# Kernel optimization log

Measured on AMD Instinct MI355X. Metric: run time of the kernel, lower is better.

Reference implementation:

```python
import jax, jax.numpy as jnp
import numpy as np

N_ATOMS = 16384
N_EDGES = 524288
N_MOL = 256
A = 4            # num_pseudo_species
S = 4            # len(unique_numbers)
NMAX = 10        # radial basis size
NSPH = 9         # (l_max+1)^2 with l_max=2
Q = A * NMAX
NL = 3           # l_max+1
F = Q * Q * NL   # 4800 power-spectrum features
CUTOFF = 5.0
AVG_ATOMS = 64.0
SCALE = 1.0
H1, H2 = 512, 512


def _sph_l012(u):
    # real spherical harmonics l=0,1,2 on unit vectors u [E,3] -> [E,9]
    x, y, z = u[:, 0], u[:, 1], u[:, 2]
    c1 = 0.4886025119029199
    c2 = 1.0925484305920792
    return jnp.stack([
        jnp.full_like(x, 0.28209479177387814),
        c1 * y, c1 * z, c1 * x,
        c2 * x * y, c2 * y * z,
        0.31539156525252005 * (3.0 * z * z - 1.0),
        c2 * x * z,
        0.5462742152960396 * (x * x - y * y),
    ], axis=-1)


def _forward(positions, cells, edge_offsets, U, gamma, beta, W1, W2, W3, Wc,
             numbers, edge_indices, batch):
    send, recv = edge_indices[0], edge_indices[1]
    cell_e = cells[batch[send]]                                  # [E,3,3]
    rvec = positions[recv] - positions[send] + jnp.einsum('ek,ekl->el', edge_offsets, cell_e)
    r = jnp.sqrt(jnp.sum(rvec * rvec, axis=-1) + 1e-12)          # [E]
    rhat = rvec / r[:, None]
    fc = 0.5 * (jnp.cos(jnp.pi * r / CUTOFF) + 1.0) * (r < CUTOFF)
    mu = jnp.linspace(0.0, CUTOFF, NMAX)
    sig = CUTOFF / NMAX
    R = jnp.exp(-((r[:, None] - mu) ** 2) / (2.0 * sig * sig)) * fc[:, None]  # [E,NMAX]
    Y = _sph_l012(rhat)                                          # [E,9]
    RY = jnp.einsum('en,ek->enk', R, Y)                          # [E,NMAX,9]
    w = U[:, numbers[send]]                                      # [A,E] pseudo-species mix of neighbor species
    # spherical expansion per atom: c[i,a,n,lm]
    c = jnp.stack([jax.ops.segment_sum(w[a][:, None, None] * RY, recv, num_segments=N_ATOMS)
                   for a in range(A)], axis=1)                   # [N,A,NMAX,9]
    c = c.reshape(N_ATOMS, Q, NSPH)
    # power spectrum: contract over m within each l block, normalize by sqrt(2l+1)
    lblocks = [(0, 1, 1.0), (1, 4, 3.0), (4, 9, 5.0)]
    ps = jnp.stack([jnp.einsum('iqm,ipm->iqp', c[:, :, a:b], c[:, :, a:b]) / jnp.sqrt(nl)
                    for a, b, nl in lblocks], axis=-1).reshape(N_ATOMS, F)
    # layer norm
    mean = ps.mean(axis=-1, keepdims=True)
    var = ps.var(axis=-1, keepdims=True)
    x = (ps - mean) / jnp.sqrt(var + 1e-5) * gamma + beta

    def contract(x, W):
        # species-indexed contraction: per-species weight via combination matrix U
        Wsp = jnp.einsum('as,aio->sio', U, W)                    # [S,in,out]
        out = jnp.zeros((x.shape[0], W.shape[-1]), x.dtype)
        for s in range(S):                                       # small fixed species set
            out = out + jnp.where((numbers == s)[:, None], x @ Wsp[s], 0.0)
        return out

    x = jax.nn.silu(contract(x, W1))
    x = jax.nn.silu(contract(x, W2))
    x = contract(x, W3)                                          # [N,1]
    e = jax.ops.segment_sum(x, batch, num_segments=N_MOL)        # [M,1]
    e = e / jnp.sqrt(float(A)) / AVG_ATOMS
    comp = jax.ops.segment_sum(jax.nn.one_hot(numbers, S, dtype=x.dtype), batch, num_segments=N_MOL)
    return e * SCALE + comp @ Wc.T


def setup_inputs() -> dict:
    key = jax.random.key(0)
    ks = jax.random.split(key, 10)
    positions = jax.random.normal(ks[0], (N_ATOMS, 3), dtype=jnp.float32)
    cells = jnp.zeros((N_MOL, 3, 3), dtype=jnp.float32)
    numbers = jax.random.randint(ks[1], (N_ATOMS,), 0, S)
    edge_indices = jax.random.randint(ks[2], (2, N_EDGES), 0, N_ATOMS)
    edge_offsets = jnp.zeros((N_EDGES, 3), dtype=jnp.float32)
    batch = jnp.sort(jax.random.randint(ks[3], (N_ATOMS,), 0, N_MOL))
    U = jax.random.normal(ks[4], (A, S), dtype=jnp.float32) * 0.5
    gamma = jnp.ones((F,), dtype=jnp.float32)
    beta = jnp.zeros((F,), dtype=jnp.float32)
    W1 = jax.random.normal(ks[5], (A, F, H1), dtype=jnp.float32) / np.sqrt(F)
    W2 = jax.random.normal(ks[6], (A, H1, H2), dtype=jnp.float32) / np.sqrt(H1)
    W3 = jax.random.normal(ks[7], (A, H2, 1), dtype=jnp.float32) / np.sqrt(H2)
    Wc = jax.random.normal(ks[8], (1, S), dtype=jnp.float32) * 0.1
    return {"positions": positions, "cells": cells, "numbers": numbers,
            "edge_indices": edge_indices, "edge_offsets": edge_offsets, "batch": batch,
            "U": U, "gamma": gamma, "beta": beta, "W1": W1, "W2": W2, "W3": W3, "Wc": Wc}


def reference(positions, cells, numbers, edge_indices, edge_offsets, batch,
              U, gamma, beta, W1, W2, W3, Wc):
    return _forward(positions, cells, edge_offsets, U, gamma, beta, W1, W2, W3, Wc,
                    numbers, edge_indices, batch)
```

## Files before the change

kernel.cpp:

```cpp
#include <hip/hip_runtime.h>

#define NA   16384
#define NE   524288
#define NM   256
#define FF   4800
#define FR   2688
#define HH   512
#define NMX  10
#define NSPH 9

typedef __bf16 bf16x8 __attribute__((ext_vector_type(8)));
typedef float  f32x4  __attribute__((ext_vector_type(4)));
typedef unsigned short u16x8 __attribute__((ext_vector_type(8)));

__device__ inline unsigned short f2bf(float x){
  unsigned int u = __builtin_bit_cast(unsigned int, x);
  u += 0x7fffu + ((u >> 16) & 1u);
  return (unsigned short)(u >> 16);
}
__device__ inline float bf2f(unsigned short h){
  unsigned int u = ((unsigned int)h) << 16;
  return __builtin_bit_cast(float, u);
}
__device__ inline void atomic_add_f(float* p, float v){
  __hip_atomic_fetch_add(p, v, __ATOMIC_RELAXED, __HIP_MEMORY_SCOPE_AGENT);
}
__device__ inline void gload16(const void* g, void* l){
  __builtin_amdgcn_global_load_lds(
      (const __attribute__((address_space(1))) unsigned int*)g,
      (__attribute__((address_space(3))) unsigned int*)l, 16, 0, 0);
}
__device__ inline float silu(float x){ return x / (1.f + __expf(-x)); }

__device__ inline void decode_blk(int b, int& qb, int& pb){
  int q = 0, rem = b;
  while (rem >= 10 - q){ rem -= 10 - q; q++; }
  qb = q; pb = q + rem;
}

template<int CNT>
__device__ inline void ps_block(const float* __restrict__ cl, int qb, int pb, int off,
                                float nrm, bool diag, unsigned short* ob,
                                float& s1, float& s2){
  float cq[4][CNT], cp[4][CNT];
  #pragma unroll
  for (int i = 0; i < 4; i++)
    #pragma unroll
    for (int k = 0; k < CNT; k++){
      cq[i][k] = cl[(qb*4 + i)*9 + off + k];
      cp[i][k] = cl[(pb*4 + i)*9 + off + k];
    }
  #pragma unroll
  for (int qi = 0; qi < 4; qi++)
    #pragma unroll
    for (int pi = 0; pi < 4; pi++){
      float v = 0.f;
      #pragma unroll
      for (int k = 0; k < CNT; k++) v += cq[qi][k] * cp[pi][k];
      v *= nrm;
      float wgt = diag ? ((qi < pi) ? 2.f : ((qi == pi) ? 1.f : 0.f)) : 2.f;
      if (diag && qi > pi) v = 0.f;
      ob[qi*4 + pi] = f2bf(v);
      s1 += wgt * v;
      s2 += wgt * v * v;
    }
}

__device__ inline int block_scan_excl(int v, int tid, int* lds){
  int lane = tid & 63, w = tid >> 6;
  int x = v;
  #pragma unroll
  for (int d = 1; d < 64; d <<= 1){
    int y = __shfl_up(x, d, 64);
    if (lane >= d) x += y;
  }
  if (lane == 63) lds[w] = x;
  __syncthreads();
  int wsum = 0;
  for (int i = 0; i < w; i++) wsum += lds[i];
  return wsum + x - v;
}

__global__ __launch_bounds__(256) void k_hist(const int* __restrict__ ei,
                                              const int* __restrict__ numbers,
                                              int* __restrict__ cnt64k){
  int e = blockIdx.x * 256 + threadIdx.x;
  if (e < NE){
    int key = ei[NE + e] * 4 + numbers[ei[e]];
    atomicAdd(&cnt64k[key], 1);
  }
}

__global__ __launch_bounds__(256) void k_scanA(const int* __restrict__ cnt64k,
                                               int* __restrict__ bsum){
  __shared__ int lds[4];
  int tid = threadIdx.x;
  int v = cnt64k[blockIdx.x * 256 + tid];
  int lane = tid & 63;
  #pragma unroll
  for (int m = 32; m; m >>= 1) v += __shfl_xor(v, m, 64);
  if (lane == 0) lds[tid >> 6] = v;
  __syncthreads();
  if (tid == 0) bsum[blockIdx.x] = lds[0] + lds[1] + lds[2] + lds[3];
}

__global__ __launch_bounds__(256) void k_scanB(const int* __restrict__ bsum,
                                               int* __restrict__ boff, int* __restrict__ starts){
  __shared__ int lds[4];
  int tid = threadIdx.x;
  int v = bsum[tid];
  int e = block_scan_excl(v, tid, lds);
  boff[tid] = e;
  if (tid == 0) starts[65536] = NE;
}

__global__ __launch_bounds__(256) void k_scanC(const int* __restrict__ cnt64k,
                                               const int* __restrict__ boff,
                                               int* __restrict__ starts, int* __restrict__ cursor){
  __shared__ int lds[4];
  int tid = threadIdx.x;
  int bin = blockIdx.x * 256 + tid;
  int v = cnt64k[bin];
  int e = block_scan_excl(v, tid, lds) + boff[blockIdx.x];
  starts[bin] = e;
  cursor[bin] = e;
}

__global__ __launch_bounds__(256) void k_sortperm(const int* __restrict__ ei,
                                                  const int* __restrict__ numbers,
                                                  int* __restrict__ cursor, int* __restrict__ perm){
  int e = blockIdx.x * 256 + threadIdx.x;
  if (e < NE){
    int key = ei[NE + e] * 4 + numbers[ei[e]];
    int p = atomicAdd(&cursor[key], 1);
    perm[p] = e;
  }
}

__global__ __launch_bounds__(256) void k_acount(const int* __restrict__ numbers,
                                                int* __restrict__ bhist){
  __shared__ int h[4];
  int tid = threadIdx.x;
  if (tid < 4) h[tid] = 0;
  __syncthreads();
  atomicAdd(&h[numbers[blockIdx.x * 256 + tid]], 1);
  __syncthreads();
  if (tid < 4) bhist[blockIdx.x * 4 + tid] = h[tid];
}

__global__ void k_aoffs(const int* __restrict__ bhist, int* __restrict__ boffs,
                        int* __restrict__ ints){
  if (threadIdx.x == 0){
    int* cnt = ints; int* offs = ints + 8;
    int tot[4] = {0,0,0,0};
    for (int b = 0; b < 64; b++)
      for (int s = 0; s < 4; s++) tot[s] += bhist[b*4 + s];
    int o = 0;
    for (int s = 0; s < 4; s++){ cnt[s] = tot[s]; offs[s] = o; o += tot[s]; }
    offs[4] = o;
    int run[4];
    for (int s = 0; s < 4; s++) run[s] = offs[s];
    for (int b = 0; b < 64; b++)
      for (int s = 0; s < 4; s++){ boffs[b*4 + s] = run[s]; run[s] += bhist[b*4 + s]; }
  }
}

__global__ __launch_bounds__(256) void k_aplace(const int* __restrict__ numbers,
                                                const int* __restrict__ boffs,
                                                int* __restrict__ list){
  __shared__ int ws[4][4];
  int tid = threadIdx.x, w = tid >> 6, lane = tid & 63;
  int i = blockIdx.x * 256 + tid;
  int sp = numbers[i];
  int rank = 0;
  #pragma unroll
  for (int s = 0; s < 4; s++){
    unsigned long long m = __ballot(sp == s);
    if (s == sp) rank = __popcll(m & (((unsigned long long)1 << lane) - 1));
    if (lane == 0) ws[w][s] = __popcll(m);
  }
  __syncthreads();
  int pre = 0;
  for (int w2 = 0; w2 < w; w2++) pre += ws[w2][sp];
  list[boffs[blockIdx.x * 4 + sp] + pre + rank] = i;
}

__global__ __launch_bounds__(384) void k_atom(
    const float* __restrict__ pos, const float* __restrict__ cells,
    const int* __restrict__ ei, const float* __restrict__ eoff,
    const int* __restrict__ batch, const int* __restrict__ startsK,
    const int* __restrict__ perm, const float* __restrict__ U,
    unsigned short* __restrict__ ps, float* __restrict__ stats)
{
  __shared__ float Rl[64][NMX];
  __shared__ float Yl[64][NSPH];
  __shared__ float csr[360];
  __shared__ float cl[360];
  __shared__ float red[16];
  __shared__ float ul[16];
  int atom = blockIdx.x;
  int tid = threadIdx.x;
  if (tid < 16) ul[tid] = U[tid];
  int e0 = startsK[atom * 4], e1 = startsK[atom * 4 + 4];
  float px = pos[atom*3+0], py = pos[atom*3+1], pz = pos[atom*3+2];
  int sp = tid / 90, n = (tid % 90) / 9, k = tid % 9;
  int aS = 0, aE = 0;
  if (tid < 360){ aS = startsK[atom * 4 + sp]; aE = startsK[atom * 4 + sp + 1]; }
  float acc = 0.f;
  for (int base = e0; base < e1; base += 64){
    int nch = min(64, e1 - base);
    if (tid < nch){
      int e = perm[base + tid];
      int snd = ei[e];
      const float* C = cells + (size_t)batch[snd] * 9;
      float o0 = eoff[e*3+0], o1 = eoff[e*3+1], o2 = eoff[e*3+2];
      float rx = px - pos[snd*3+0] + o0*C[0] + o1*C[3] + o2*C[6];
      float ry = py - pos[snd*3+1] + o0*C[1] + o1*C[4] + o2*C[7];
      float rz = pz - pos[snd*3+2] + o0*C[2] + o1*C[5] + o2*C[8];
      float r = sqrtf(rx*rx + ry*ry + rz*rz + 1e-12f);
      float inv = 1.f / r;
      float hx = rx*inv, hy = ry*inv, hz = rz*inv;
      float fc = (r < 5.f) ? (0.5f * (__cosf(r * 0.6283185307179586f) + 1.f)) : 0.f;
      #pragma unroll
      for (int nn = 0; nn < NMX; nn++){
        float d = r - (5.f/9.f) * (float)nn;
        Rl[tid][nn] = __expf(-2.f * d * d) * fc;
      }
      Yl[tid][0] = 0.28209479177387814f;
      Yl[tid][1] = 0.4886025119029199f * hy;
      Yl[tid][2] = 0.4886025119029199f * hz;
      Yl[tid][3] = 0.4886025119029199f * hx;
      Yl[tid][4] = 1.0925484305920792f * hx * hy;
      Yl[tid][5] = 1.0925484305920792f * hy * hz;
      Yl[tid][6] = 0.31539156525252005f * (3.f * hz * hz - 1.f);
      Yl[tid][7] = 1.0925484305920792f * hx * hz;
      Yl[tid][8] = 0.5462742152960396f * (hx * hx - hy * hy);
    }
    __syncthreads();
    if (tid < 360){
      int lo2 = max(aS, base), hi2 = min(aE, base + nch);
      for (int e = lo2; e < hi2; e++){
        int j = e - base;
        acc += Rl[j][n] * Yl[j][k];
      }
    }
    __syncthreads();
  }
  if (tid < 360) csr[tid] = acc;
  __syncthreads();
  if (tid < 360){
    int a = tid / 90, nk = tid % 90;
    cl[tid] = ul[a*4+0]*csr[nk] + ul[a*4+1]*csr[90+nk]
            + ul[a*4+2]*csr[180+nk] + ul[a*4+3]*csr[270+nk];
  }
  __syncthreads();
  float s1 = 0.f, s2 = 0.f;
  int l = tid >> 6, b = tid & 63;
  if (l < 3 && b < 55){
    int qb, pb;
    decode_blk(b, qb, pb);
    bool diag = (qb == pb);
    unsigned short ob[16];
    if (l == 0)      ps_block<1>(cl, qb, pb, 0, 1.f, diag, ob, s1, s2);
    else if (l == 1) ps_block<3>(cl, qb, pb, 1, 0.5773502691896258f, diag, ob, s1, s2);
    else             ps_block<5>(cl, qb, pb, 4, 0.4472135954999579f, diag, ob, s1, s2);
    unsigned short* dst = ps + (size_t)atom * FR + b * 48 + l * 16;
    *reinterpret_cast<u16x8*>(dst)     = *(const u16x8*)&ob[0];
    *reinterpret_cast<u16x8*>(dst + 8) = *(const u16x8*)&ob[8];
  } else if (tid >= 192 && tid < 198){
    unsigned short zb[8] = {0,0,0,0,0,0,0,0};
    *reinterpret_cast<u16x8*>(ps + (size_t)atom * FR + 2640 + (tid - 192) * 8) = *(const u16x8*)zb;
  }
  #pragma unroll
  for (int m = 32; m; m >>= 1){ s1 += __shfl_xor(s1, m, 64); s2 += __shfl_xor(s2, m, 64); }
  int w = tid >> 6, lane = tid & 63;
  if (lane == 0){ red[w] = s1; red[8 + w] = s2; }
  __syncthreads();
  if (tid == 0){
    float t1 = 0.f, t2 = 0.f;
    for (int i = 0; i < 6; i++){ t1 += red[i]; t2 += red[8 + i]; }
    float mean = t1 * (1.f / FF);
    float var = t2 * (1.f / FF) - mean * mean;
    var = fmaxf(var, 0.f);
    stats[2*atom]   = mean;
    stats[2*atom+1] = rsqrtf(var + 1e-5f);
  }
}

__global__ __launch_bounds__(256) void k_wg1(
    const float* __restrict__ W1, const float* __restrict__ U,
    const float* __restrict__ gamma, const float* __restrict__ beta,
    unsigned short* __restrict__ Wg, float* __restrict__ gW, float* __restrict__ bW)
{
  __shared__ float tg[64][65];
  __shared__ float tb[64][65];
  int n0 = blockIdx.x * 64, f0 = blockIdx.y * 64, s = blockIdx.z;
  float u0 = U[s], u1 = U[4+s], u2 = U[8+s], u3 = U[12+s];
  int tid = threadIdx.x;
  #pragma unroll 4
  for (int rep = 0; rep < 16; rep++){
    int idx = rep * 256 + tid;
    int fi = idx >> 6, ni = idx & 63;
    int fp = f0 + fi;
    int b = fp / 48, r = fp % 48;
    int l = r >> 4, qi = (r >> 2) & 3, pi = r & 3;
    float tgv = 0.f, tbv = 0.f;
    if (b < 55){
      int qb, pb;
      decode_blk(b, qb, pb);
      bool zero = (qb == pb) && (qi > pi);
      if (!zero){
        int q = qb*4 + qi, p = pb*4 + pi;
        int fa = (q * 40 + p) * 3 + l;
        size_t basea = (size_t)fa * 512 + (n0 + ni);
        float wa = u0*W1[basea] + u1*W1[basea + (size_t)FF*512]
                 + u2*W1[basea + (size_t)2*FF*512] + u3*W1[basea + (size_t)3*FF*512];
        tgv = gamma[fa] * wa;
        tbv = beta[fa] * wa;
        if (p != q){
          int fb = (p * 40 + q) * 3 + l;
          size_t baseb = (size_t)fb * 512 + (n0 + ni);
          float wb = u0*W1[baseb] + u1*W1[baseb + (size_t)FF*512]
                   + u2*W1[baseb + (size_t)2*FF*512] + u3*W1[baseb + (size_t)3*FF*512];
          tgv += gamma[fb] * wb;
          tbv += beta[fb] * wb;
        }
      }
    }
    tg[fi][ni] = tgv;
    tb[fi][ni] = tbv;
  }
  __syncthreads();
  #pragma unroll 4
  for (int rep = 0; rep < 16; rep++){
    int idx = rep * 256 + tid;
    int ni = idx >> 6, fi = idx & 63;
    Wg[((size_t)s * 512 + n0 + ni) * FR + f0 + fi] = f2bf(tg[fi][ni]);
  }
  if (tid < 64){
    float sg = 0.f, sb = 0.f;
    for (int fi = 0; fi < 64; fi++){ sg += tg[fi][tid]; sb += tb[fi][tid]; }
    atomic_add_f(&gW[s * 512 + n0 + tid], sg);
    atomic_add_f(&bW[s * 512 + n0 + tid], sb);
  }
}

__global__ __launch_bounds__(256) void k_w2t(
    const float* __restrict__ W2, const float* __restrict__ U,
    unsigned short* __restrict__ W2t)
{
  __shared__ float t[64][65];
  int n0 = blockIdx.x * 64, k0 = blockIdx.y * 64, s = blockIdx.z;
  float u0 = U[s], u1 = U[4+s], u2 = U[8+s], u3 = U[12+s];
  int tid = threadIdx.x;
  #pragma unroll 4
  for (int rep = 0; rep < 16; rep++){
    int idx = rep * 256 + tid;
    int ki = idx >> 6, ni = idx & 63;
    size_t base = (size_t)(k0 + ki) * 512 + (n0 + ni);
    t[ki][ni] = u0*W2[base] + u1*W2[base + 512*512]
              + u2*W2[base + 2*512*512] + u3*W2[base + 3*512*512];
  }
  __syncthreads();
  #pragma unroll 4
  for (int rep = 0; rep < 16; rep++){
    int idx = rep * 256 + tid;
    int ni = idx >> 6, ki = idx & 63;
    W2t[((size_t)s * 512 + n0 + ni) * 512 + k0 + ki] = f2bf(t[ki][ni]);
  }
}

__global__ void k_w3(const float* __restrict__ W3, const float* __restrict__ U,
                     float* __restrict__ W3s)
{
  int idx = blockIdx.x * 256 + threadIdx.x;
  if (idx < 4 * 512){
    int s = idx >> 9, k = idx & 511;
    W3s[idx] = U[s]*W3[k] + U[4+s]*W3[512+k] + U[8+s]*W3[2*512+k] + U[12+s]*W3[3*512+k];
  }
}

template<int EPI, int NSPLIT>
__global__ __launch_bounds__(256) void k_gemm(
    const unsigned short* __restrict__ Ag, int lda, int K,
    const unsigned short* __restrict__ Btg,
    const int* __restrict__ list, const int* __restrict__ offs, const int* __restrict__ cnt,
    unsigned short* __restrict__ pout,
    const float* __restrict__ W3s, float* __restrict__ pacc)
{
  __shared__ alignas(16) char smem[32768];
  const int NV = 4 * NSPLIT;
  int b = blockIdx.x;
  int y = (b & 7) + 8 * (b / (8 * NV));
  int v = (b >> 3) % NV;
  int x = v & 3, kh = v >> 2;

  int s = 0, t = y;
  for (; s < 4; s++){
    int nts = (cnt[s] + 127) >> 7;
    if (t < nts) break;
    t -= nts;
  }
  if (s >= 4) return;
  int cntS = cnt[s], offS = offs[s];
  int rt = t, n0 = x * 128;
  int tid = threadIdx.x, w = tid >> 6, lane = tid & 63;
  int wr = w >> 1, wc = w & 1;

  const unsigned short* Bts = Btg + (size_t)s * 512 * K;
  const unsigned short* gA[4];
  const unsigned short* gB[4];
  char* lA[4];
  char* lB[4];
  #pragma unroll
  for (int it = 0; it < 4; it++){
    int g = it * 4 + w;
    int idx = g * 64 + lane;
    int row = idx >> 3, ch = idx & 7;
    int cg = ch ^ (row & 7);
    int gr = rt * 128 + row; gr = gr < cntS ? gr : cntS - 1;
    int atom = list[offS + gr];
    gA[it] = Ag + (size_t)atom * lda + cg * 8;
    lA[it] = smem + g * 1024;
    gB[it] = Bts + (size_t)(n0 + row) * K + cg * 8;
    lB[it] = smem + 16384 + g * 1024;
  }

  int hi = lane >> 4, lo = lane & 15;
  f32x4 acc[4][4];
  #pragma unroll
  for (int mi = 0; mi < 4; mi++)
    #pragma unroll
    for (int ni = 0; ni < 4; ni++)
      #pragma unroll
      for (int r = 0; r < 4; r++) acc[mi][ni][r] = 0.f;

  int abase[4], a7[4], bbase[4], b7[4];
  #pragma unroll
  for (int mi = 0; mi < 4; mi++){ int row = wr*64 + mi*16 + lo; abase[mi] = row*128; a7[mi] = row & 7; }
  #pragma unroll
  for (int ni = 0; ni < 4; ni++){ int row = wc*64 + ni*16 + lo; bbase[ni] = 16384 + row*128; b7[ni] = row & 7; }

  int nk = K / 64;
  int k0 = ((nk * kh) / NSPLIT) * 64;
  int k1 = ((nk * (kh + 1)) / NSPLIT) * 64;

  for (int kt = k0; kt < k1; kt += 64){
    #pragma unroll
    for (int it = 0; it < 4; it++) gload16(gA[it] + kt, lA[it]);
    #pragma unroll
    for (int it = 0; it < 4; it++) gload16(gB[it] + kt, lB[it]);
    __syncthreads();
    #pragma unroll
    for (int kk = 0; kk < 2; kk++){
      bf16x8 af[4], bfr[4];
      #pragma unroll
      for (int mi = 0; mi < 4; mi++)
        af[mi] = *(const bf16x8*)(smem + abase[mi] + (((kk*4 + hi) ^ a7[mi]) << 4));
      #pragma unroll
      for (int ni = 0; ni < 4; ni++)
        bfr[ni] = *(const bf16x8*)(smem + bbase[ni] + (((kk*4 + hi) ^ b7[ni]) << 4));
      #pragma unroll
      for (int mi = 0; mi < 4; mi++)
        #pragma unroll
        for (int ni = 0; ni < 4; ni++)
          acc[mi][ni] = __builtin_amdgcn_mfma_f32_16x16x32_bf16(af[mi], bfr[ni], acc[mi][ni], 0, 0, 0);
    }
    __syncthreads();
  }

  int gn[4];
  #pragma unroll
  for (int ni = 0; ni < 4; ni++) gn[ni] = n0 + wc*64 + ni*16 + lo;

  if (EPI == 0){
    #pragma unroll
    for (int mi = 0; mi < 4; mi++){
      #pragma unroll
      for (int j = 0; j < 4; j++){
        int gr = rt*128 + wr*64 + mi*16 + hi*4 + j;
        if (gr < cntS){
          int atom = list[offS + gr];
          #pragma unroll
          for (int ni = 0; ni < 4; ni++)
            pout[((size_t)kh * NA + atom) * 512 + gn[ni]] = f2bf(acc[mi][ni][j]);
        }
      }
    }
  } else {
    float w3v[4];
    #pragma unroll
    for (int ni = 0; ni < 4; ni++) w3v[ni] = W3s[s * 512 + gn[ni]];
    float* pslot = pacc + (size_t)(x * 2 + wc) * NA;
    #pragma unroll
    for (int mi = 0; mi < 4; mi++){
      #pragma unroll
      for (int j = 0; j < 4; j++){
        int gr = rt*128 + wr*64 + mi*16 + hi*4 + j;
        if (gr < cntS){
          int atom = list[offS + gr];
          float pdot = 0.f;
          #pragma unroll
          for (int ni = 0; ni < 4; ni++)
            pdot += silu(acc[mi][ni][j]) * w3v[ni];
          pdot += __shfl_xor(pdot, 1, 16);
          pdot += __shfl_xor(pdot, 2, 16);
          pdot += __shfl_xor(pdot, 4, 16);
          pdot += __shfl_xor(pdot, 8, 16);
          if (lo == 0) pslot[atom] = pdot;
        }
      }
    }
  }
}

__global__ __launch_bounds__(256) void k_epi(
    const unsigned short* __restrict__ pbuf, const float* __restrict__ stats,
    const float* __restrict__ gW, const float* __restrict__ bW,
    const int* __restrict__ numbers, unsigned short* __restrict__ h1)
{
  int w = threadIdx.x >> 6, lane = threadIdx.x & 63;
  int atom = blockIdx.x * 4 + w;
  int s = numbers[atom];
  float mean = stats[2*atom], rstd = stats[2*atom+1];
  int c0 = lane * 8;
  u16x8 a0 = *reinterpret_cast<const u16x8*>(pbuf + (size_t)atom * 512 + c0);
  u16x8 a1 = *reinterpret_cast<const u16x8*>(pbuf + (size_t)(NA + atom) * 512 + c0);
  unsigned short o[8];
  #pragma unroll
  for (int j = 0; j < 8; j++){
    int c = c0 + j;
    float acc = bf2f(a0[j]) + bf2f(a1[j]);
    float vv = rstd * acc + bW[s*512 + c] - mean * rstd * gW[s*512 + c];
    o[j] = f2bf(silu(vv));
  }
  *reinterpret_cast<u16x8*>(h1 + (size_t)atom * 512 + c0) = *(const u16x8*)o;
}

__global__ __launch_bounds__(256) void k_final2(
    const float* __restrict__ pacc, const int* __restrict__ numbers,
    const int* __restrict__ batch, const float* __restrict__ Wc,
    float* __restrict__ molOut)
{
  int atom = blockIdx.x * 256 + threadIdx.x;
  int lane = threadIdx.x & 63;
  float sum = 0.f;
  #pragma unroll
  for (int p = 0; p < 8; p++) sum += pacc[(size_t)p * NA + atom];
  float val = sum * (1.f / 128.f) + Wc[numbers[atom]];
  int mol = batch[atom];
  int m0 = __shfl(mol, 0, 64);
  int m63 = __shfl(mol, 63, 64);
  if (m0 == m63){
    #pragma unroll
    for (int m = 32; m; m >>= 1) val += __shfl_xor(val, m, 64);
    if (lane == 0) atomic_add_f(&molOut[mol], val);
  } else {
    atomic_add_f(&molOut[mol], val);
  }
}

extern "C" void kernel_launch(void* const* d_in, const int* in_sizes, int n_in,
                              void* d_out, int out_size, void* d_ws, size_t ws_size,
                              hipStream_t stream)
{
  const float* pos     = (const float*)d_in[0];
  const float* cells   = (const float*)d_in[1];
  const int*   numbers = (const int*)d_in[2];
  const int*   ei      = (const int*)d_in[3];
  const float* eoff    = (const float*)d_in[4];
  const int*   batch   = (const int*)d_in[5];
  const float* U       = (const float*)d_in[6];
  const float* gamma   = (const float*)d_in[7];
  const float* beta    = (const float*)d_in[8];
  const float* W1      = (const float*)d_in[9];
  const float* W2      = (const float*)d_in[10];
  const float* W3      = (const float*)d_in[11];
  const float* Wc      = (const float*)d_in[12];
  float* out = (float*)d_out;

  char* ws = (char*)d_ws;
  size_t off = 0;
  auto alloc = [&](size_t bytes) -> void* {
    void* p = ws + off;
    off += (bytes + 255) & ~(size_t)255;
    return p;
  };
  unsigned short* ps   = (unsigned short*)alloc((size_t)NA * FR * 2);
  unsigned short* pbuf = (unsigned short*)alloc((size_t)2 * NA * 512 * 2);
  float* stats         = (float*)alloc((size_t)NA * 2 * 4);
  unsigned short* Wg1  = (unsigned short*)alloc((size_t)4 * 512 * FR * 2);
  float* gW            = (float*)alloc(4 * 512 * 4);
  float* bW            = (float*)alloc(4 * 512 * 4);
  unsigned short* W2t  = (unsigned short*)alloc((size_t)4 * 512 * 512 * 2);
  float* W3s           = (float*)alloc(4 * 512 * 4);
  unsigned short* h1   = (unsigned short*)alloc((size_t)NA * 512 * 2);
  float* pacc          = (float*)alloc((size_t)8 * NA * 4);
  int* list            = (int*)alloc(NA * 4);
  int* perm            = (int*)alloc((size_t)NE * 4);
  int* startsK         = (int*)alloc((65536 + 1) * 4);
  int* cnt64k          = (int*)alloc(65536 * 4);
  int* cursor64k       = (int*)alloc(65536 * 4);
  int* bsum            = (int*)alloc(256 * 4);
  int* boff            = (int*)alloc(256 * 4);
  int* bhist           = (int*)alloc(64 * 4 * 4);
  int* boffs           = (int*)alloc(64 * 4 * 4);
  int* ints            = (int*)alloc(64);
  int* cnt = ints; int* offs = ints + 8;

  hipMemsetAsync(cnt64k, 0, 65536 * 4, stream);
  hipMemsetAsync(gW, 0, 4 * 512 * 4, stream);
  hipMemsetAsync(bW, 0, 4 * 512 * 4, stream);
  hipMemsetAsync(out, 0, (size_t)out_size * 4, stream);

  k_hist<<<NE / 256, 256, 0, stream>>>(ei, numbers, cnt64k);
  k_scanA<<<256, 256, 0, stream>>>(cnt64k, bsum);
  k_scanB<<<1, 256, 0, stream>>>(bsum, boff, startsK);
  k_scanC<<<256, 256, 0, stream>>>(cnt64k, boff, startsK, cursor64k);
  k_sortperm<<<NE / 256, 256, 0, stream>>>(ei, numbers, cursor64k, perm);

  k_acount<<<NA / 256, 256, 0, stream>>>(numbers, bhist);
  k_aoffs<<<1, 64, 0, stream>>>(bhist, boffs, ints);
  k_aplace<<<NA / 256, 256, 0, stream>>>(numbers, boffs, list);

  k_atom<<<NA, 384, 0, stream>>>(pos, cells, ei, eoff, batch, startsK, perm, U, ps, stats);

  k_wg1<<<dim3(8, 42, 4), 256, 0, stream>>>(W1, U, gamma, beta, Wg1, gW, bW);
  k_w2t<<<dim3(8, 8, 4), 256, 0, stream>>>(W2, U, W2t);
  k_w3<<<8, 256, 0, stream>>>(W3, U, W3s);

  k_gemm<0, 2><<<1088, 256, 0, stream>>>(ps, FR, FR, Wg1, list, offs, cnt,
                                         pbuf, nullptr, nullptr);
  k_epi<<<NA / 4, 256, 0, stream>>>(pbuf, stats, gW, bW, numbers, h1);

  k_gemm<2, 1><<<544, 256, 0, stream>>>(h1, 512, 512, W2t, list, offs, cnt,
                                        nullptr, W3s, pacc);
  k_final2<<<NA / 256, 256, 0, stream>>>(pacc, numbers, batch, Wc, out);
}
```

Baseline: 331.4 us.

## Fuse W1 prep across species, raise GEMM1 split-K to four, merge memsets

The W1 weight-prep kernel now processes all four species in one block. It reads each W1 element once instead of four times and writes the transposed bf16 tile with vectorised 16-byte stores. The first GEMM raises its split-K factor from 2 to 4, doubling the grid to 2176 blocks for better occupancy, and the epilogue now sums four partial buffers. The gW/bW buffers are moved next to cnt64k so that a single memset clears all three. Costs are a larger partial-sum buffer, extra epilogue traffic and extra bf16 rounding of partial sums.

New measurement: 326.1 us. No clear change (-1.6%).

```diff
diff --git a/kernel.cpp b/kernel.cpp
--- a/kernel.cpp
+++ b/kernel.cpp
@@ -287,24 +287,26 @@
   }
 }
 
-__global__ __launch_bounds__(256) void k_wg1(
+__global__ __launch_bounds__(256) void k_wg3(
     const float* __restrict__ W1, const float* __restrict__ U,
     const float* __restrict__ gamma, const float* __restrict__ beta,
     unsigned short* __restrict__ Wg, float* __restrict__ gW, float* __restrict__ bW)
 {
-  __shared__ float tg[64][65];
-  __shared__ float tb[64][65];
-  int n0 = blockIdx.x * 64, f0 = blockIdx.y * 64, s = blockIdx.z;
-  float u0 = U[s], u1 = U[4+s], u2 = U[8+s], u3 = U[12+s];
-  int tid = threadIdx.x;
-  #pragma unroll 4
+  __shared__ unsigned short og[4][64][64];
+  int n0 = blockIdx.x * 64, f0 = blockIdx.y * 64;
+  int tid = threadIdx.x, ni = tid & 63;
+  float u[4][4];
+  #pragma unroll
+  for (int a = 0; a < 4; a++)
+    #pragma unroll
+    for (int s = 0; s < 4; s++) u[a][s] = U[a*4 + s];
+  float gs[4] = {0,0,0,0}, bs[4] = {0,0,0,0};
   for (int rep = 0; rep < 16; rep++){
-    int idx = rep * 256 + tid;
-    int fi = idx >> 6, ni = idx & 63;
+    int fi = rep * 4 + (tid >> 6);
     int fp = f0 + fi;
     int b = fp / 48, r = fp % 48;
     int l = r >> 4, qi = (r >> 2) & 3, pi = r & 3;
-    float tgv = 0.f, tbv = 0.f;
+    float tg[4] = {0,0,0,0}, tb[4] = {0,0,0,0};
     if (b < 55){
       int qb, pb;
       decode_blk(b, qb, pb);
@@ -312,36 +314,53 @@
       if (!zero){
         int q = qb*4 + qi, p = pb*4 + pi;
         int fa = (q * 40 + p) * 3 + l;
-        size_t basea = (size_t)fa * 512 + (n0 + ni);
-        float wa = u0*W1[basea] + u1*W1[basea + (size_t)FF*512]
-                 + u2*W1[basea + (size_t)2*FF*512] + u3*W1[basea + (size_t)3*FF*512];
-        tgv = gamma[fa] * wa;
-        tbv = beta[fa] * wa;
+        float ga = gamma[fa], ba = beta[fa];
+        float wm[4] = {0,0,0,0};
+        #pragma unroll
+        for (int a = 0; a < 4; a++){
+          float wa = W1[(size_t)a * FF * 512 + (size_t)fa * 512 + n0 + ni];
+          #pragma unroll
+          for (int s = 0; s < 4; s++) wm[s] += u[a][s] * wa;
+        }
+        #pragma unroll
+        for (int s = 0; s < 4; s++){ tg[s] = ga * wm[s]; tb[s] = ba * wm[s]; }
         if (p != q){
           int fb = (p * 40 + q) * 3 + l;
-          size_t baseb = (size_t)fb * 512 + (n0 + ni);
-          float wb = u0*W1[baseb] + u1*W1[baseb + (size_t)FF*512]
-                   + u2*W1[baseb + (size_t)2*FF*512] + u3*W1[baseb + (size_t)3*FF*512];
-          tgv += gamma[fb] * wb;
-          tbv += beta[fb] * wb;
+          float gb = gamma[fb], bb = beta[fb];
+          float wn[4] = {0,0,0,0};
+          #pragma unroll
+          for (int a = 0; a < 4; a++){
+            float wb = W1[(size_t)a * FF * 512 + (size_t)fb * 512 + n0 + ni];
+            #pragma unroll
+            for (int s = 0; s < 4; s++) wn[s] += u[a][s] * wb;
+          }
+          #pragma unroll
+          for (int s = 0; s < 4; s++){ tg[s] += gb * wn[s]; tb[s] += bb * wn[s]; }
         }
       }
     }
-    tg[fi][ni] = tgv;
-    tb[fi][ni] = tbv;
-  }
-  __syncthreads();
-  #pragma unroll 4
-  for (int rep = 0; rep < 16; rep++){
-    int idx = rep * 256 + tid;
-    int ni = idx >> 6, fi = idx & 63;
-    Wg[((size_t)s * 512 + n0 + ni) * FR + f0 + fi] = f2bf(tg[fi][ni]);
-  }
-  if (tid < 64){
-    float sg = 0.f, sb = 0.f;
-    for (int fi = 0; fi < 64; fi++){ sg += tg[fi][tid]; sb += tb[fi][tid]; }
-    atomic_add_f(&gW[s * 512 + n0 + tid], sg);
-    atomic_add_f(&bW[s * 512 + n0 + tid], sb);
+    #pragma unroll
+    for (int s = 0; s < 4; s++){
+      og[s][fi][ni] = f2bf(tg[s]);
+      gs[s] += tg[s];
+      bs[s] += tb[s];
+    }
+  }
+  #pragma unroll
+  for (int s = 0; s < 4; s++){
+    atomic_add_f(&gW[s * 512 + n0 + ni], gs[s]);
+    atomic_add_f(&bW[s * 512 + n0 + ni], bs[s]);
+  }
+  __syncthreads();
+  for (int it = 0; it < 8; it++){
+    int idx = it * 256 + tid;
+    int c = idx & 7;
+    int rrow = idx >> 3;
+    int s = rrow >> 6, nn = rrow & 63;
+    unsigned short o[8];
+    #pragma unroll
+    for (int j = 0; j < 8; j++) o[j] = og[s][c*8 + j][nn];
+    *reinterpret_cast<u16x8*>(&Wg[((size_t)s * 512 + n0 + nn) * FR + f0 + c * 8]) = *(const u16x8*)o;
   }
 }
 
@@ -526,11 +545,13 @@
   int c0 = lane * 8;
   u16x8 a0 = *reinterpret_cast<const u16x8*>(pbuf + (size_t)atom * 512 + c0);
   u16x8 a1 = *reinterpret_cast<const u16x8*>(pbuf + (size_t)(NA + atom) * 512 + c0);
+  u16x8 a2 = *reinterpret_cast<const u16x8*>(pbuf + (size_t)(2*NA + atom) * 512 + c0);
+  u16x8 a3 = *reinterpret_cast<const u16x8*>(pbuf + (size_t)(3*NA + atom) * 512 + c0);
   unsigned short o[8];
   #pragma unroll
   for (int j = 0; j < 8; j++){
     int c = c0 + j;
-    float acc = bf2f(a0[j]) + bf2f(a1[j]);
+    float acc = (bf2f(a0[j]) + bf2f(a1[j])) + (bf2f(a2[j]) + bf2f(a3[j]));
     float vv = rstd * acc + bW[s*512 + c] - mean * rstd * gW[s*512 + c];
     o[j] = f2bf(silu(vv));
   }
@@ -587,11 +608,9 @@
     return p;
   };
   unsigned short* ps   = (unsigned short*)alloc((size_t)NA * FR * 2);
-  unsigned short* pbuf = (unsigned short*)alloc((size_t)2 * NA * 512 * 2);
+  unsigned short* pbuf = (unsigned short*)alloc((size_t)4 * NA * 512 * 2);
   float* stats         = (float*)alloc((size_t)NA * 2 * 4);
   unsigned short* Wg1  = (unsigned short*)alloc((size_t)4 * 512 * FR * 2);
-  float* gW            = (float*)alloc(4 * 512 * 4);
-  float* bW            = (float*)alloc(4 * 512 * 4);
   unsigned short* W2t  = (unsigned short*)alloc((size_t)4 * 512 * 512 * 2);
   float* W3s           = (float*)alloc(4 * 512 * 4);
   unsigned short* h1   = (unsigned short*)alloc((size_t)NA * 512 * 2);
@@ -600,6 +619,8 @@
   int* perm            = (int*)alloc((size_t)NE * 4);
   int* startsK         = (int*)alloc((65536 + 1) * 4);
   int* cnt64k          = (int*)alloc(65536 * 4);
+  float* gW            = (float*)alloc(4 * 512 * 4);
+  float* bW            = (float*)alloc(4 * 512 * 4);
   int* cursor64k       = (int*)alloc(65536 * 4);
   int* bsum            = (int*)alloc(256 * 4);
   int* boff            = (int*)alloc(256 * 4);
@@ -608,9 +629,7 @@
   int* ints            = (int*)alloc(64);
   int* cnt = ints; int* offs = ints + 8;
 
-  hipMemsetAsync(cnt64k, 0, 65536 * 4, stream);
-  hipMemsetAsync(gW, 0, 4 * 512 * 4, stream);
-  hipMemsetAsync(bW, 0, 4 * 512 * 4, stream);
+  hipMemsetAsync(cnt64k, 0, 65536 * 4 + 2 * 4 * 512 * 4, stream);
   hipMemsetAsync(out, 0, (size_t)out_size * 4, stream);
 
   k_hist<<<NE / 256, 256, 0, stream>>>(ei, numbers, cnt64k);
@@ -625,11 +644,11 @@
 
   k_atom<<<NA, 384, 0, stream>>>(pos, cells, ei, eoff, batch, startsK, perm, U, ps, stats);
 
-  k_wg1<<<dim3(8, 42, 4), 256, 0, stream>>>(W1, U, gamma, beta, Wg1, gW, bW);
+  k_wg3<<<dim3(8, 42), 256, 0, stream>>>(W1, U, gamma, beta, Wg1, gW, bW);
   k_w2t<<<dim3(8, 8, 4), 256, 0, stream>>>(W2, U, W2t);
   k_w3<<<8, 256, 0, stream>>>(W3, U, W3s);
 
-  k_gemm<0, 2><<<1088, 256, 0, stream>>>(ps, FR, FR, Wg1, list, offs, cnt,
+  k_gemm<0, 4><<<2176, 256, 0, stream>>>(ps, FR, FR, Wg1, list, offs, cnt,
                                          pbuf, nullptr, nullptr);
   k_epi<<<NA / 4, 256, 0, stream>>>(pbuf, stats, gW, bW, numbers, h1);
 
```
